# Kernel tuning notes

Measured on AMD Instinct MI355X. Metric: run time of the kernel, lower is better.

Reference implementation:

```python
import jax, jax.numpy as jnp
import numpy as np
import math

D_IN = 1024
D_OUT = 1024
NUM_HEADS = 16
HEAD_DIM = D_OUT // NUM_HEADS
B = 2
S = 4096


def setup_inputs() -> dict:
    key = jax.random.key(0)
    ks = jax.random.split(key, 6)
    x = jax.random.normal(ks[0], (B, S, D_IN), dtype=jnp.float32)
    # kaiming-uniform-ish scale for weights; exact init values don't matter for correctness
    bound = 1.0 / math.sqrt(D_IN)
    Wq = jax.random.uniform(ks[1], (D_OUT, D_IN), minval=-bound, maxval=bound, dtype=jnp.float32)
    Wk = jax.random.uniform(ks[2], (D_OUT, D_IN), minval=-bound, maxval=bound, dtype=jnp.float32)
    Wv = jax.random.uniform(ks[3], (D_OUT, D_IN), minval=-bound, maxval=bound, dtype=jnp.float32)
    Wo = jax.random.uniform(ks[4], (D_OUT, D_OUT), minval=-bound, maxval=bound, dtype=jnp.float32)
    bo = jax.random.uniform(ks[5], (D_OUT,), minval=-bound, maxval=bound, dtype=jnp.float32)
    return {"x": x, "Wq": Wq, "Wk": Wk, "Wv": Wv, "Wo": Wo, "bo": bo}


@jax.custom_vjp
def binarize(w):
    return jnp.sign(w)

def _bin_fwd(w):
    return jnp.sign(w), w

def _bin_bwd(w, g):
    # straight-through estimator: pass grad where |w| <= 1
    return (g * (jnp.abs(w) <= 1).astype(g.dtype),)

binarize.defvjp(_bin_fwd, _bin_bwd)


def reference(x, Wq, Wk, Wv, Wo, bo):
    b, n, _ = x.shape
    h, hd = NUM_HEADS, HEAD_DIM
    # binarized projections (torch F.linear: x @ W.T)
    q = (x @ binarize(Wq).T).reshape(b, n, h, hd).transpose(0, 2, 1, 3)  # [b,h,n,hd]
    k = (x @ binarize(Wk).T).reshape(b, n, h, hd).transpose(0, 2, 1, 3)
    v = (x @ binarize(Wv).T).reshape(b, n, h, hd).transpose(0, 2, 1, 3)
    scores = jnp.einsum('bhqd,bhkd->bhqk', q, k) / math.sqrt(hd)  # [b,h,n,n]
    causal = jnp.tril(jnp.ones((n, n), dtype=bool))
    scores = jnp.where(causal, scores, -jnp.inf)
    attn = jax.nn.softmax(scores, axis=-1)
    # dropout p=0.0 -> identity
    ctx = jnp.einsum('bhqk,bhkd->bqhd', attn, v).reshape(b, n, h * hd)
    return ctx @ binarize(Wo).T + bo
```

## Files before the change

### kernel.cpp

```cpp
#include <hip/hip_runtime.h>
#include <hip/hip_bf16.h>
#include <cstdint>
#include <cstddef>

#define S 4096
#define D 1024
#define H 16
#define HD 64
#define BATCH 2
#define M_TOK 8192
#define K2 2048

typedef short short8 __attribute__((ext_vector_type(8)));
typedef __bf16 bf16x8 __attribute__((ext_vector_type(8)));
typedef float f32x4 __attribute__((ext_vector_type(4)));
typedef unsigned int u32;

static __device__ __forceinline__ ushort f2bf(float f) {
  union { float f; uint32_t u; } v; v.f = f;
  uint32_t u = v.u + 0x7FFFu + ((v.u >> 16) & 1u);
  return (ushort)(u >> 16);
}
static __device__ __forceinline__ float bf2f(ushort h) {
  union { uint32_t u; float f; } v; v.u = ((uint32_t)h) << 16; return v.f;
}
static __device__ __forceinline__ uint32_t cvtpk(float lo, float hi) {
  uint32_t r;
  asm("v_cvt_pk_bf16_f32 %0, %1, %2" : "=v"(r) : "v"(lo), "v"(hi));
  return r;
}
static __device__ __forceinline__ float vexp2(float x) {
  float r;
  asm("v_exp_f32 %0, %1" : "=v"(r) : "v"(x));
  return r;
}
static __device__ __forceinline__ bf16x8 pack4(uint32_t a, uint32_t b, uint32_t c, uint32_t d) {
  union { uint32_t u[4]; bf16x8 v; } z;
  z.u[0] = a; z.u[1] = b; z.u[2] = c; z.u[3] = d;
  return z.v;
}
static __device__ __forceinline__ void gld16(const void* g, void* l) {
  __builtin_amdgcn_global_load_lds(
      (const __attribute__((address_space(1))) u32*)g,
      (__attribute__((address_space(3))) u32*)l, 16, 0, 0);
}
static __device__ __forceinline__ ushort sgn(float a) {
  return a > 0.f ? 0x3F80 : (a < 0.f ? 0xBF80 : 0);
}

__global__ void prep_x(const float* __restrict__ x, ushort* __restrict__ xcat) {
  int i = blockIdx.x * blockDim.x + threadIdx.x;
  const int total = M_TOK * 128;
  for (; i < total; i += gridDim.x * blockDim.x) {
    int row = i >> 7, c8 = (i & 127) * 8;
    const float* px = &x[(size_t)row * 1024 + c8];
    float4 a = *(const float4*)px;
    float4 b = *(const float4*)(px + 4);
    float va[8] = {a.x, a.y, a.z, a.w, b.x, b.y, b.z, b.w};
    union { ushort u[8]; short8 v; } Hh, Ll;
#pragma unroll
    for (int j = 0; j < 8; ++j) {
      ushort h = f2bf(va[j]);
      Hh.u[j] = h;
      Ll.u[j] = f2bf(va[j] - bf2f(h));
    }
    *(short8*)&xcat[(size_t)row * K2 + c8] = Hh.v;
    *(short8*)&xcat[(size_t)row * K2 + 1024 + c8] = Ll.v;
  }
}

__global__ void prep_w(const float* __restrict__ wq, const float* __restrict__ wk,
                       const float* __restrict__ wv, const float* __restrict__ wo,
                       ushort* __restrict__ wcat, ushort* __restrict__ wob) {
  int i = blockIdx.x * blockDim.x + threadIdx.x;
  const int total = (D * D) / 4;
  for (; i < total; i += gridDim.x * blockDim.x) {
    float4 a;
    union { ushort u[4]; uint2 v; } t;
    a = *(const float4*)&wq[i * 4];
    t.u[0] = sgn(a.x); t.u[1] = sgn(a.y); t.u[2] = sgn(a.z); t.u[3] = sgn(a.w);
    *(uint2*)&wcat[i * 4] = t.v;
    a = *(const float4*)&wk[i * 4];
    t.u[0] = sgn(a.x); t.u[1] = sgn(a.y); t.u[2] = sgn(a.z); t.u[3] = sgn(a.w);
    *(uint2*)&wcat[D * D + i * 4] = t.v;
    a = *(const float4*)&wv[i * 4];
    t.u[0] = sgn(a.x); t.u[1] = sgn(a.y); t.u[2] = sgn(a.z); t.u[3] = sgn(a.w);
    *(uint2*)&wcat[2 * D * D + i * 4] = t.v;
    a = *(const float4*)&wo[i * 4];
    t.u[0] = sgn(a.x); t.u[1] = sgn(a.y); t.u[2] = sgn(a.z); t.u[3] = sgn(a.w);
    *(uint2*)&wob[i * 4] = t.v;
  }
}

template<int EPI, int KK, int BROW>
__global__ __launch_bounds__(256) void gemm97(
    const ushort* __restrict__ A, const ushort* __restrict__ Bw,
    ushort* __restrict__ q_hi, ushort* __restrict__ q_lo,
    ushort* __restrict__ k_hi, ushort* __restrict__ k_lo,
    ushort* __restrict__ v_t,
    float* __restrict__ of, const float* __restrict__ bias)
{
  __shared__ ushort smA[128 * 32];
  __shared__ ushort smB[128 * 32];
  const int tid = threadIdx.x;
  const int l = tid & 63;
  const int w = tid >> 6;
  const int x = l & 15, g = l >> 4;
  const int wm = w >> 1, wn = w & 1;
  const int bm = blockIdx.x, bn = blockIdx.y;

  const ushort* gA[2]; const ushort* gB[2]; int ldso[2];
#pragma unroll
  for (int p = 0; p < 2; ++p) {
    int q = p * 256 + tid;
    gA[p] = &A[(size_t)(bm * 128 + (q >> 2)) * KK + (q & 3) * 8];
    gB[p] = &Bw[(size_t)(bn * 128 + (q >> 2)) * BROW + (q & 3) * 8];
    ldso[p] = (p * 256 + w * 64) * 8;
  }

  f32x4 acc[4][4] = {};

  for (int k0 = 0; k0 < KK; k0 += 32) {
    __syncthreads();
#pragma unroll
    for (int p = 0; p < 2; ++p) {
      gld16(gA[p] + k0, &smA[ldso[p]]);
      gld16(gB[p] + (k0 & (BROW - 1)), &smB[ldso[p]]);
    }
    __syncthreads();
    bf16x8 af[4], bf_[4];
#pragma unroll
    for (int m = 0; m < 4; ++m)
      af[m] = *(const bf16x8*)&smA[(wm * 64 + m * 16 + x) * 32 + g * 8];
#pragma unroll
    for (int n = 0; n < 4; ++n)
      bf_[n] = *(const bf16x8*)&smB[(wn * 64 + n * 16 + x) * 32 + g * 8];
#pragma unroll
    for (int m = 0; m < 4; ++m)
#pragma unroll
      for (int n = 0; n < 4; ++n)
        acc[m][n] = __builtin_amdgcn_mfma_f32_16x16x32_bf16(af[m], bf_[n], acc[m][n], 0, 0, 0);
  }

  if (EPI == 0) {
    const int proj = bn >> 3;
    ushort* oh = (proj == 0) ? q_hi : k_hi;
    ushort* ol = (proj == 0) ? q_lo : k_lo;
#pragma unroll
    for (int m = 0; m < 4; ++m)
#pragma unroll
      for (int n = 0; n < 4; ++n)
#pragma unroll
        for (int r = 0; r < 4; ++r) {
          int rowg = bm * 128 + wm * 64 + m * 16 + g * 4 + r;
          int colg = bn * 128 + wn * 64 + n * 16 + x;
          float v = acc[m][n][r];
          int bi = rowg >> 12, ntok = rowg & 4095;
          int cg = colg & 1023;
          int h = cg >> 6, hd = cg & 63;
          size_t bhb = (size_t)(bi * H + h) * (S * HD);
          if (proj < 2) {
            size_t off = bhb + (size_t)ntok * HD + hd;
            ushort hiv = f2bf(v);
            oh[off] = hiv;
            ol[off] = f2bf(v - bf2f(hiv));
          } else {
            int t5 = ntok & 31;
            int pos = ((t5 >> 2) & 3) * 8 + ((t5 >> 4) & 1) * 4 + (t5 & 3);
            v_t[bhb + (size_t)hd * S + (ntok & ~31) + pos] = f2bf(v);
          }
        }
  } else {
#pragma unroll
    for (int m = 0; m < 4; ++m)
#pragma unroll
      for (int n = 0; n < 4; ++n)
#pragma unroll
        for (int r = 0; r < 4; ++r) {
          int rowg = bm * 128 + wm * 64 + m * 16 + g * 4 + r;
          int colg = bn * 128 + wn * 64 + n * 16 + x;
          of[(size_t)rowg * D + colg] = acc[m][n][r] + bias[colg];
        }
  }
}

__global__ __launch_bounds__(256) void flash5(
    const ushort* __restrict__ qhi, const ushort* __restrict__ qlo,
    const ushort* __restrict__ khi, const ushort* __restrict__ klo,
    const ushort* __restrict__ vt, ushort* __restrict__ ctx)
{
  __shared__ ushort smKhi[2][64 * 64];
  __shared__ ushort smKlo[2][64 * 64];
  __shared__ ushort smVT[2][64 * 64];

  const int tid = threadIdx.x;
  const int l = tid & 63;
  const int w = tid >> 6;
  const int x = l & 15;
  const int g = l >> 4;
  const int bh = blockIdx.x;
  const int qt = (int)(gridDim.y - 1) - (int)blockIdx.y;
  const int qbase = qt * 128;
  const size_t qkbase = (size_t)bh * S * HD;

  int soff_k[2]; size_t soff_v[2]; int ldso[2];
#pragma unroll
  for (int p = 0; p < 2; ++p) {
    int q = p * 256 + tid;
    int rr = q >> 3;
    int sb = (q & 7) ^ (rr & 7);
    soff_k[p] = rr * HD + sb * 8;
    soff_v[p] = (size_t)rr * S + sb * 8;
    ldso[p] = (p * 256 + w * 64) * 8;
  }
  const ushort* khb = khi + qkbase;
  const ushort* klb = klo + qkbase;
  const ushort* vtb = vt + qkbase;

  bf16x8 bq[2][2][2];
#pragma unroll
  for (int qs = 0; qs < 2; ++qs) {
    int qrow = qbase + w * 32 + qs * 16 + x;
    size_t base = qkbase + (size_t)qrow * HD + g * 8;
    bq[qs][0][0] = *(const bf16x8*)&qhi[base];
    bq[qs][0][1] = *(const bf16x8*)&qhi[base + 32];
    bq[qs][1][0] = *(const bf16x8*)&qlo[base];
    bq[qs][1][1] = *(const bf16x8*)&qlo[base + 32];
  }

  float mrun[2] = {-1e30f, -1e30f};
  float lrun[2] = {0.f, 0.f};
  f32x4 oacc[2][4] = {};

  const int kvmax = (qbase + 127) >> 6;
  const int qmaxw = qbase + w * 32 + 31;
  const float C1 = 0.125f * 1.44269504f;
  const float TH = 8.0f / C1;

#pragma unroll
  for (int p = 0; p < 2; ++p) {
    gld16(khb + soff_k[p], &smKhi[0][ldso[p]]);
    gld16(klb + soff_k[p], &smKlo[0][ldso[p]]);
    gld16(vtb + soff_v[p], &smVT[0][ldso[p]]);
  }
  __syncthreads();

  int cur = 0;
  for (int kv = 0; kv <= kvmax; ++kv) {
    if (kv < kvmax) {
      const ushort* kh = khb + (size_t)(kv + 1) * (64 * HD);
      const ushort* kl = klb + (size_t)(kv + 1) * (64 * HD);
      const ushort* vp = vtb + (size_t)(kv + 1) * 64;
      int nb = cur ^ 1;
#pragma unroll
      for (int p = 0; p < 2; ++p) {
        gld16(kh + soff_k[p], &smKhi[nb][ldso[p]]);
        gld16(kl + soff_k[p], &smKlo[nb][ldso[p]]);
        gld16(vp + soff_v[p], &smVT[nb][ldso[p]]);
      }
    }

    if (kv * 64 <= qmaxw) {
      const ushort* bKhi = smKhi[cur];
      const ushort* bKlo = smKlo[cur];
      const ushort* bVT = smVT[cur];

      f32x4 scq[2][4];
      __builtin_amdgcn_s_setprio(1);
#pragma unroll
      for (int t = 0; t < 4; ++t) {
        f32x4 a0 = {}, a1 = {};
#pragma unroll
        for (int c = 0; c < 2; ++c) {
          int pb = (t * 16 + x) * 64 + ((4 * c + g) ^ (x & 7)) * 8;
          bf16x8 kH = *(const bf16x8*)&bKhi[pb];
          bf16x8 kL = *(const bf16x8*)&bKlo[pb];
          a0 = __builtin_amdgcn_mfma_f32_16x16x32_bf16(kH, bq[0][0][c], a0, 0, 0, 0);
          a0 = __builtin_amdgcn_mfma_f32_16x16x32_bf16(kL, bq[0][0][c], a0, 0, 0, 0);
          a0 = __builtin_amdgcn_mfma_f32_16x16x32_bf16(kH, bq[0][1][c], a0, 0, 0, 0);
          a1 = __builtin_amdgcn_mfma_f32_16x16x32_bf16(kH, bq[1][0][c], a1, 0, 0, 0);
          a1 = __builtin_amdgcn_mfma_f32_16x16x32_bf16(kL, bq[1][0][c], a1, 0, 0, 0);
          a1 = __builtin_amdgcn_mfma_f32_16x16x32_bf16(kH, bq[1][1][c], a1, 0, 0, 0);
        }
        scq[0][t] = a0; scq[1][t] = a1;
      }
      __builtin_amdgcn_s_setprio(0);

      const bool needmask = (kv * 64 + 63 > qbase + w * 32);
      uint32_t pbq[2][2][4];

#pragma unroll
      for (int qs = 0; qs < 2; ++qs) {
        if (needmask) {
          int qglob = qbase + w * 32 + qs * 16 + x;
          int kb = kv * 64 + 4 * g;
#pragma unroll
          for (int t = 0; t < 4; ++t)
#pragma unroll
            for (int r = 0; r < 4; ++r)
              if (kb + t * 16 + r > qglob) scq[qs][t][r] = -1e30f;
        }
        float mt[4];
#pragma unroll
        for (int t = 0; t < 4; ++t)
          mt[t] = fmaxf(fmaxf(scq[qs][t][0], scq[qs][t][1]),
                        fmaxf(scq[qs][t][2], scq[qs][t][3]));
        float mloc = fmaxf(fmaxf(mt[0], mt[1]), fmaxf(mt[2], mt[3]));
        if (__any(mloc > mrun[qs] + TH)) {
          mloc = fmaxf(mloc, __shfl_xor(mloc, 16));
          mloc = fmaxf(mloc, __shfl_xor(mloc, 32));
          float mnew = fmaxf(mrun[qs], mloc);
          float scal = vexp2((mrun[qs] - mnew) * C1);
          mrun[qs] = mnew;
          lrun[qs] *= scal;
#pragma unroll
          for (int dt = 0; dt < 4; ++dt) oacc[qs][dt] *= scal;
        }
        float mc = mrun[qs] * C1;
#pragma unroll
        for (int t = 0; t < 4; ++t)
#pragma unroll
          for (int r = 0; r < 4; ++r)
            scq[qs][t][r] = vexp2(scq[qs][t][r] * C1 - mc);
        float st[4];
#pragma unroll
        for (int t = 0; t < 4; ++t)
          st[t] = (scq[qs][t][0] + scq[qs][t][1]) + (scq[qs][t][2] + scq[qs][t][3]);
        lrun[qs] += (st[0] + st[1]) + (st[2] + st[3]);
#pragma unroll
        for (int c = 0; c < 2; ++c) {
          pbq[qs][c][0] = cvtpk(scq[qs][2 * c][0], scq[qs][2 * c][1]);
          pbq[qs][c][1] = cvtpk(scq[qs][2 * c][2], scq[qs][2 * c][3]);
          pbq[qs][c][2] = cvtpk(scq[qs][2 * c + 1][0], scq[qs][2 * c + 1][1]);
          pbq[qs][c][3] = cvtpk(scq[qs][2 * c + 1][2], scq[qs][2 * c + 1][3]);
        }
      }

      __builtin_amdgcn_s_setprio(1);
#pragma unroll
      for (int c = 0; c < 2; ++c)
#pragma unroll
        for (int dt = 0; dt < 4; ++dt) {
          bf16x8 vf = *(const bf16x8*)&bVT[(dt * 16 + x) * 64 + ((4 * c + g) ^ (x & 7)) * 8];
          oacc[0][dt] = __builtin_amdgcn_mfma_f32_16x16x32_bf16(
              vf, pack4(pbq[0][c][0], pbq[0][c][1], pbq[0][c][2], pbq[0][c][3]), oacc[0][dt], 0, 0, 0);
          oacc[1][dt] = __builtin_amdgcn_mfma_f32_16x16x32_bf16(
              vf, pack4(pbq[1][c][0], pbq[1][c][1], pbq[1][c][2], pbq[1][c][3]), oacc[1][dt], 0, 0, 0);
        }
      __builtin_amdgcn_s_setprio(0);
    }

    __syncthreads();
    cur ^= 1;
  }

  const int b = bh >> 4, h = bh & 15;
#pragma unroll
  for (int qs = 0; qs < 2; ++qs) {
    float ls = lrun[qs];
    ls += __shfl_xor(ls, 16);
    ls += __shfl_xor(ls, 32);
    float inv = 1.0f / ls;
    int tok = qbase + w * 32 + qs * 16 + x;
#pragma unroll
    for (int dt = 0; dt < 4; ++dt) {
      uint2 uu;
      uu.x = cvtpk(oacc[qs][dt][0] * inv, oacc[qs][dt][1] * inv);
      uu.y = cvtpk(oacc[qs][dt][2] * inv, oacc[qs][dt][3] * inv);
      *(uint2*)&ctx[(size_t)(b * S + tok) * D + h * 64 + dt * 16 + 4 * g] = uu;
    }
  }
}

extern "C" void kernel_launch(void* const* d_in, const int* in_sizes, int n_in,
                              void* d_out, int out_size, void* d_ws, size_t ws_size,
                              hipStream_t stream) {
  const float* x  = (const float*)d_in[0];
  const float* Wq = (const float*)d_in[1];
  const float* Wk = (const float*)d_in[2];
  const float* Wv = (const float*)d_in[3];
  const float* Wo = (const float*)d_in[4];
  const float* bo = (const float*)d_in[5];
  float* out = (float*)d_out;

  if (ws_size < (size_t)120 * 1024 * 1024) return;

  char* ws = (char*)d_ws;
  const size_t MB = 1024 * 1024;
  ushort* xcat = (ushort*)(ws);
  ushort* ctx  = (ushort*)(ws);
  ushort* wcat = (ushort*)(ws + 32 * MB);
  ushort* wob  = (ushort*)(ws + 38 * MB);
  ushort* qhi  = (ushort*)(ws + 40 * MB);
  ushort* qlo  = (ushort*)(ws + 56 * MB);
  ushort* khi  = (ushort*)(ws + 72 * MB);
  ushort* klo  = (ushort*)(ws + 88 * MB);
  ushort* vt   = (ushort*)(ws + 104 * MB);

  prep_x<<<2048, 256, 0, stream>>>(x, xcat);
  prep_w<<<1024, 256, 0, stream>>>(Wq, Wk, Wv, Wo, wcat, wob);

  gemm97<0, K2, 1024><<<dim3(64, 24), 256, 0, stream>>>(
      xcat, wcat, qhi, qlo, khi, klo, vt, nullptr, nullptr);

  flash5<<<dim3(BATCH * H, S / 128), 256, 0, stream>>>(qhi, qlo, khi, klo, vt, ctx);

  gemm97<2, 1024, 1024><<<dim3(64, 8), 256, 0, stream>>>(
      ctx, wob, nullptr, nullptr, nullptr, nullptr, nullptr, out, bo);
}
```

Before: 339.3 us.

## Split QKV projection into pipelined 256x256 QK GEMM and hi-only V GEMM

Q and K now come from a new 256x256-tile GEMM with 512 threads and a triple-buffered LDS pipeline. It uses swizzled shared-memory layout, partial vmcnt waits and setprio around the MFMA block. V is computed by a separate 128-tile GEMM that reads only the first 1024 columns of the split-x buffer, which halves its reduction depth. This targets better data reuse and overlap of loads with compute in the dominant projection. The cost is a second launch, higher LDS use that limits occupancy, and slightly lower V precision from dropping the low-order x part.

Result: faster. 324.3 us (-4.4%).

```diff
diff --git a/kernel.cpp b/kernel.cpp
--- a/kernel.cpp
+++ b/kernel.cpp
@@ -92,11 +92,110 @@
   }
 }
 
-template<int EPI, int KK, int BROW>
+__global__ __launch_bounds__(512, 2) void gemm256(
+    const ushort* __restrict__ A, const ushort* __restrict__ Bw,
+    ushort* __restrict__ q_hi, ushort* __restrict__ q_lo,
+    ushort* __restrict__ k_hi, ushort* __restrict__ k_lo)
+{
+  __shared__ ushort smA[3][256 * 32];
+  __shared__ ushort smB[3][256 * 32];
+  const int tid = threadIdx.x;
+  const int l = tid & 63;
+  const int w = tid >> 6;
+  const int x = l & 15, g = l >> 4;
+  const int wm = w >> 2, wn = w & 3;
+  const int bm = blockIdx.x, bn = blockIdx.y;
+
+  const ushort* gA[2]; const ushort* gB[2]; int ldso[2];
+#pragma unroll
+  for (int r = 0; r < 2; ++r) {
+    int q = r * 512 + tid;
+    int row = q >> 2;
+    int blk = (q & 3) ^ ((row & 3) ^ ((row >> 2) & 3));
+    gA[r] = &A[(size_t)(bm * 256 + row) * 2048 + blk * 8];
+    gB[r] = &Bw[(size_t)(bn * 256 + row) * 1024 + blk * 8];
+    ldso[r] = (r * 512 + w * 64) * 8;
+  }
+
+  f32x4 acc[8][4] = {};
+
+#pragma unroll
+  for (int r = 0; r < 2; ++r) {
+    gld16(gA[r] + 0, &smA[0][ldso[r]]);
+    gld16(gB[r] + 0, &smB[0][ldso[r]]);
+  }
+#pragma unroll
+  for (int r = 0; r < 2; ++r) {
+    gld16(gA[r] + 32, &smA[1][ldso[r]]);
+    gld16(gB[r] + ((32) & 1023), &smB[1][ldso[r]]);
+  }
+
+  const int swz = (x & 3) ^ ((x >> 2) & 3);
+  int cb = 0;
+  for (int s = 0; s < 64; ++s) {
+    if (s < 63) {
+      asm volatile("s_waitcnt vmcnt(4)" ::: "memory");
+    } else {
+      asm volatile("s_waitcnt vmcnt(0)" ::: "memory");
+    }
+    __builtin_amdgcn_s_barrier();
+
+    if (s + 2 < 64) {
+      int nb = cb - 1; if (nb < 0) nb = 2;
+      int k0 = (s + 2) * 32;
+#pragma unroll
+      for (int r = 0; r < 2; ++r) {
+        gld16(gA[r] + k0, &smA[nb][ldso[r]]);
+        gld16(gB[r] + (k0 & 1023), &smB[nb][ldso[r]]);
+      }
+    }
+
+    const ushort* bA = smA[cb];
+    const ushort* bB = smB[cb];
+    bf16x8 af[8], bf_[4];
+#pragma unroll
+    for (int m = 0; m < 8; ++m)
+      af[m] = *(const bf16x8*)&bA[(wm * 128 + m * 16 + x) * 32 + (g ^ swz) * 8];
+#pragma unroll
+    for (int n = 0; n < 4; ++n)
+      bf_[n] = *(const bf16x8*)&bB[(wn * 64 + n * 16 + x) * 32 + (g ^ swz) * 8];
+
+    __builtin_amdgcn_s_setprio(1);
+#pragma unroll
+    for (int m = 0; m < 8; ++m)
+#pragma unroll
+      for (int n = 0; n < 4; ++n)
+        acc[m][n] = __builtin_amdgcn_mfma_f32_16x16x32_bf16(af[m], bf_[n], acc[m][n], 0, 0, 0);
+    __builtin_amdgcn_s_setprio(0);
+
+    cb = (cb == 2) ? 0 : cb + 1;
+  }
+
+#pragma unroll
+  for (int m = 0; m < 8; ++m)
+#pragma unroll
+    for (int n = 0; n < 4; ++n)
+#pragma unroll
+      for (int r = 0; r < 4; ++r) {
+        int rowg = bm * 256 + wm * 128 + m * 16 + g * 4 + r;
+        int colg = bn * 256 + wn * 64 + n * 16 + x;
+        float v = acc[m][n][r];
+        int bi = rowg >> 12, ntok = rowg & 4095;
+        int proj = colg >> 10;
+        int cg = colg & 1023;
+        int h = cg >> 6, hd = cg & 63;
+        ushort* oh = (proj == 0) ? q_hi : k_hi;
+        ushort* ol = (proj == 0) ? q_lo : k_lo;
+        size_t off = (size_t)(bi * H + h) * (S * HD) + (size_t)ntok * HD + hd;
+        ushort hiv = f2bf(v);
+        oh[off] = hiv;
+        ol[off] = f2bf(v - bf2f(hiv));
+      }
+}
+
+template<int EPI, int KK, int BROW, int AST>
 __global__ __launch_bounds__(256) void gemm97(
     const ushort* __restrict__ A, const ushort* __restrict__ Bw,
-    ushort* __restrict__ q_hi, ushort* __restrict__ q_lo,
-    ushort* __restrict__ k_hi, ushort* __restrict__ k_lo,
     ushort* __restrict__ v_t,
     float* __restrict__ of, const float* __restrict__ bias)
 {
@@ -113,7 +212,7 @@
 #pragma unroll
   for (int p = 0; p < 2; ++p) {
     int q = p * 256 + tid;
-    gA[p] = &A[(size_t)(bm * 128 + (q >> 2)) * KK + (q & 3) * 8];
+    gA[p] = &A[(size_t)(bm * 128 + (q >> 2)) * AST + (q & 3) * 8];
     gB[p] = &Bw[(size_t)(bn * 128 + (q >> 2)) * BROW + (q & 3) * 8];
     ldso[p] = (p * 256 + w * 64) * 8;
   }
@@ -142,46 +241,27 @@
         acc[m][n] = __builtin_amdgcn_mfma_f32_16x16x32_bf16(af[m], bf_[n], acc[m][n], 0, 0, 0);
   }
 
-  if (EPI == 0) {
-    const int proj = bn >> 3;
-    ushort* oh = (proj == 0) ? q_hi : k_hi;
-    ushort* ol = (proj == 0) ? q_lo : k_lo;
-#pragma unroll
-    for (int m = 0; m < 4; ++m)
-#pragma unroll
-      for (int n = 0; n < 4; ++n)
-#pragma unroll
-        for (int r = 0; r < 4; ++r) {
-          int rowg = bm * 128 + wm * 64 + m * 16 + g * 4 + r;
-          int colg = bn * 128 + wn * 64 + n * 16 + x;
-          float v = acc[m][n][r];
+#pragma unroll
+  for (int m = 0; m < 4; ++m)
+#pragma unroll
+    for (int n = 0; n < 4; ++n)
+#pragma unroll
+      for (int r = 0; r < 4; ++r) {
+        int rowg = bm * 128 + wm * 64 + m * 16 + g * 4 + r;
+        int colg = bn * 128 + wn * 64 + n * 16 + x;
+        float v = acc[m][n][r];
+        if (EPI == 2) {
+          of[(size_t)rowg * D + colg] = v + bias[colg];
+        } else {
           int bi = rowg >> 12, ntok = rowg & 4095;
           int cg = colg & 1023;
           int h = cg >> 6, hd = cg & 63;
           size_t bhb = (size_t)(bi * H + h) * (S * HD);
-          if (proj < 2) {
-            size_t off = bhb + (size_t)ntok * HD + hd;
-            ushort hiv = f2bf(v);
-            oh[off] = hiv;
-            ol[off] = f2bf(v - bf2f(hiv));
-          } else {
-            int t5 = ntok & 31;
-            int pos = ((t5 >> 2) & 3) * 8 + ((t5 >> 4) & 1) * 4 + (t5 & 3);
-            v_t[bhb + (size_t)hd * S + (ntok & ~31) + pos] = f2bf(v);
-          }
-        }
-  } else {
-#pragma unroll
-    for (int m = 0; m < 4; ++m)
-#pragma unroll
-      for (int n = 0; n < 4; ++n)
-#pragma unroll
-        for (int r = 0; r < 4; ++r) {
-          int rowg = bm * 128 + wm * 64 + m * 16 + g * 4 + r;
-          int colg = bn * 128 + wn * 64 + n * 16 + x;
-          of[(size_t)rowg * D + colg] = acc[m][n][r] + bias[colg];
-        }
-  }
+          int t5 = ntok & 31;
+          int pos = ((t5 >> 2) & 3) * 8 + ((t5 >> 4) & 1) * 4 + (t5 & 3);
+          v_t[bhb + (size_t)hd * S + (ntok & ~31) + pos] = f2bf(v);
+        }
+      }
 }
 
 __global__ __launch_bounds__(256) void flash5(
@@ -207,10 +287,10 @@
 #pragma unroll
   for (int p = 0; p < 2; ++p) {
     int q = p * 256 + tid;
-    int rr = q >> 3;
-    int sb = (q & 7) ^ (rr & 7);
-    soff_k[p] = rr * HD + sb * 8;
-    soff_v[p] = (size_t)rr * S + sb * 8;
+    int r2 = q >> 3;
+    int sb = (q & 7) ^ (r2 & 7);
+    soff_k[p] = r2 * HD + sb * 8;
+    soff_v[p] = (size_t)r2 * S + sb * 8;
     ldso[p] = (p * 256 + w * 64) * 8;
   }
   const ushort* khb = khi + qkbase;
@@ -400,11 +480,12 @@
   prep_x<<<2048, 256, 0, stream>>>(x, xcat);
   prep_w<<<1024, 256, 0, stream>>>(Wq, Wk, Wv, Wo, wcat, wob);
 
-  gemm97<0, K2, 1024><<<dim3(64, 24), 256, 0, stream>>>(
-      xcat, wcat, qhi, qlo, khi, klo, vt, nullptr, nullptr);
+  gemm256<<<dim3(32, 8), 512, 0, stream>>>(xcat, wcat, qhi, qlo, khi, klo);
+  gemm97<1, 1024, 1024, 2048><<<dim3(64, 8), 256, 0, stream>>>(
+      xcat, wcat + 2 * D * D, vt, nullptr, nullptr);
 
   flash5<<<dim3(BATCH * H, S / 128), 256, 0, stream>>>(qhi, qlo, khi, klo, vt, ctx);
 
-  gemm97<2, 1024, 1024><<<dim3(64, 8), 256, 0, stream>>>(
-      ctx, wob, nullptr, nullptr, nullptr, nullptr, nullptr, out, bo);
-}
+  gemm97<2, 1024, 1024, 1024><<<dim3(64, 8), 256, 0, stream>>>(
+      ctx, wob, nullptr, out, bo);
+}
```
